# Optimization experiments

Hardware: AMD Instinct MI355X
Metric: run time of the kernel (lower is better)

The kernel has to match this reference:

```python
import jax, jax.numpy as jnp
import numpy as np

N_NODES = 50000
N_EDGES = 1_250_000
D_IN = 64
D_OUT = 64


def setup_inputs() -> dict:
    key = jax.random.key(0)
    k1, k2, k3, k4, k5 = jax.random.split(key, 5)
    feature = jax.random.normal(k1, (N_NODES, D_IN), dtype=jnp.float32)
    src = jax.random.randint(k2, (N_EDGES,), 0, N_NODES, dtype=jnp.int32)
    dst = jax.random.randint(k3, (N_EDGES,), 0, N_NODES, dtype=jnp.int32)
    W = jax.random.normal(k4, (D_OUT, D_IN), dtype=jnp.float32) * (1.0 / np.sqrt(D_IN))
    b = jax.random.normal(k5, (D_OUT,), dtype=jnp.float32) * 0.01
    return {"feature": feature, "src": src, "dst": dst, "W": W, "b": b}


def reference(feature, src, dst, W, b):
    # copy_u + sum: for each edge, message = feature[src]; reduce-sum at dst.
    msgs = feature[src]                                  # [E, D_IN] irregular gather
    h = jax.ops.segment_sum(msgs, dst, num_segments=N_NODES)  # [N, D_IN] scatter-add
    return h @ W.T + b                                   # nn.Linear
```

## Files before the change

### kernel.cpp

```cpp
#include <hip/hip_runtime.h>

#define D 64
#define SNB 256
#define CVB 128
#define NBP 1024
#define SCAP 5120
#define SLOTN 4608
#define GPAD 16
#define SLCAP 2048
#define VALID_LIM (1u<<22)
#define SCAN_CHUNK 1024

static __device__ __forceinline__ unsigned short f2bf(float f) {
    unsigned u = __float_as_uint(f);
    unsigned r = (u + 0x7FFFu + ((u >> 16) & 1u)) >> 16;
    return (unsigned short)r;
}
static __device__ __forceinline__ float bf2f(unsigned short h) {
    return __uint_as_float((unsigned)h << 16);
}

__global__ void __launch_bounds__(1024)
build2_kernel(const int* __restrict__ src, const int* __restrict__ dst,
              int* __restrict__ gcur, unsigned* __restrict__ pairs,
              const float* __restrict__ feature, unsigned short* __restrict__ fbf,
              int n_edges, int nb, int chunk, int n4) {
    if (blockIdx.x >= SNB) {
        int i = (blockIdx.x - SNB) * 1024 + threadIdx.x;
        for (; i < n4; i += CVB * 1024) {
            float4 v = ((const float4*)feature)[i];
            ushort4 r;
            r.x = f2bf(v.x); r.y = f2bf(v.y); r.z = f2bf(v.z); r.w = f2bf(v.w);
            ((ushort4*)fbf)[i] = r;
        }
        return;
    }

    __shared__ unsigned inb[SCAP];
    __shared__ unsigned sortedb[SCAP];
    __shared__ int hist[NBP];
    __shared__ int cur[NBP];
    __shared__ int dlt[NBP];
    __shared__ int pstart[NBP];
    __shared__ int pcnt[NBP];
    __shared__ int wsum[16];

    int blk = blockIdx.x, tid = threadIdx.x;
    int lane = tid & 63, w = tid >> 6;

    for (int i = tid; i < NBP; i += 1024) hist[i] = 0;
    __syncthreads();

    int e0 = blk * chunk;
    int e1 = e0 + chunk; if (e1 > n_edges) e1 = n_edges;
    int m = e1 - e0;

    for (int i = tid; i < m; i += 1024) {
        int d_ = dst[e0 + i];
        int s_ = src[e0 + i];
        inb[i] = ((unsigned)(d_ >> 6) << 22) | ((unsigned)(d_ & 63) << 16) | (unsigned)s_;
        atomicAdd(&hist[d_ >> 6], 1);
    }
    __syncthreads();

    int v = hist[tid];
    int x = v;
    for (int o = 1; o < 64; o <<= 1) {
        int y = __shfl_up(x, o, 64);
        if (lane >= o) x += y;
    }
    if (lane == 63) wsum[w] = x;
    __syncthreads();
    int pre = 0;
    for (int i = 0; i < w; ++i) pre += wsum[i];
    int excl = x - v + pre;
    cur[tid] = excl;
    if (tid < nb) {
        int res = (v + 15) & ~15;
        int gb = 0, okv = 0;
        if (v > 0) {
            gb = atomicAdd(&gcur[tid * GPAD], res);
            okv = (gb + res <= SLOTN) ? 1 : 0;
        }
        int bbase = tid * SLOTN;
        dlt[tid]    = okv ? (bbase + gb - excl) : (int)0x80000000;
        pstart[tid] = bbase + gb + v;
        pcnt[tid]   = okv ? (res - v) : 0;
    }
    __syncthreads();

    for (int i = tid; i < m; i += 1024) {
        unsigned p = inb[i];
        int pos = atomicAdd(&cur[p >> 22], 1);
        sortedb[pos] = p;
    }
    __syncthreads();

    for (int i = tid; i < m; i += 1024) {
        unsigned t = sortedb[i];
        int dl = dlt[t >> 22];
        if (dl != (int)0x80000000) pairs[dl + i] = t & 0x3FFFFFu;
    }
    for (int b = tid; b < nb; b += 1024) {
        int p0 = pstart[b], n = pcnt[b];
        for (int i = 0; i < n; ++i) pairs[p0 + i] = 0xFFFFFFFFu;
    }
}

__global__ void __launch_bounds__(1024, 8)
agg3_kernel(const unsigned short* __restrict__ fbf,
            const unsigned* __restrict__ pairs,
            const int* __restrict__ gcur,
            const float* __restrict__ W,
            const float* __restrict__ bias,
            float* __restrict__ out, int n_nodes) {
    __shared__ float4 Wt4[64 * 16];
    __shared__ float  H[64 * 65];
    __shared__ unsigned short slist[SLCAP];
    __shared__ int cnt[64], offs[64], cur[64];

    int tid = threadIdx.x;
    int lane = tid & 63, w = tid >> 6;
    int g = lane >> 4, sl = lane & 15;

    {   int k = tid >> 4, oq = tid & 15;
        float4 v;
        v.x = W[(4 * oq + 0) * 64 + k];
        v.y = W[(4 * oq + 1) * 64 + k];
        v.z = W[(4 * oq + 2) * 64 + k];
        v.w = W[(4 * oq + 3) * 64 + k];
        Wt4[k * 16 + oq] = v;
    }

    int bkt = blockIdx.x;
    int len = gcur[bkt * GPAD]; if (len > SLOTN) len = SLOTN;
    int e0 = bkt * SLOTN;

    if (tid < 64) cnt[tid] = 0;
    __syncthreads();
    for (int i = tid; i < len; i += 1024) {
        unsigned p = pairs[e0 + i];
        if (p < VALID_LIM) atomicAdd(&cnt[p >> 16], 1);
    }
    __syncthreads();
    if (w == 0) {
        int v = cnt[lane];
        int x = v;
        for (int o = 1; o < 64; o <<= 1) {
            int y = __shfl_up(x, o, 64);
            if (lane >= o) x += y;
        }
        offs[lane] = x - v; cur[lane] = x - v;
    }
    __syncthreads();
    for (int i = tid; i < len; i += 1024) {
        unsigned p = pairs[e0 + i];
        if (p < VALID_LIM) {
            int pos = atomicAdd(&cur[p >> 16], 1);
            if (pos < SLCAP) slist[pos] = (unsigned short)(p & 0xffffu);
        }
    }
    __syncthreads();

    int offq[4], dq[4];
#pragma unroll
    for (int q = 0; q < 4; ++q) {
        int ln = w + q * 16;
        offq[q] = offs[ln];
        dq[q] = cnt[ln];
    }
    int dmax = dq[0];
    if (dq[1] > dmax) dmax = dq[1];
    if (dq[2] > dmax) dmax = dq[2];
    if (dq[3] > dmax) dmax = dq[3];

    float4 a4[4];
#pragma unroll
    for (int q = 0; q < 4; ++q) { a4[q].x = a4[q].y = a4[q].z = a4[q].w = 0.f; }

    for (int j = 0; j < dmax; j += 4) {
        ushort4 u[4];
        float msk[4];
#pragma unroll
        for (int q = 0; q < 4; ++q) {
            int i0 = j + g;
            int d = dq[q];
            int ic = (i0 < d) ? i0 : ((d > 0) ? d - 1 : 0);
            int s = slist[offq[q] + ic];
            u[q] = *(const ushort4*)(fbf + s * D + sl * 4);
            msk[q] = (i0 < d) ? 1.f : 0.f;
        }
#pragma unroll
        for (int q = 0; q < 4; ++q) {
            a4[q].x += bf2f(u[q].x) * msk[q];
            a4[q].y += bf2f(u[q].y) * msk[q];
            a4[q].z += bf2f(u[q].z) * msk[q];
            a4[q].w += bf2f(u[q].w) * msk[q];
        }
    }

#pragma unroll
    for (int q = 0; q < 4; ++q) {
        float4 h = a4[q];
        h.x += __shfl_xor(h.x, 16, 64);  h.y += __shfl_xor(h.y, 16, 64);
        h.z += __shfl_xor(h.z, 16, 64);  h.w += __shfl_xor(h.w, 16, 64);
        h.x += __shfl_xor(h.x, 32, 64);  h.y += __shfl_xor(h.y, 32, 64);
        h.z += __shfl_xor(h.z, 32, 64);  h.w += __shfl_xor(h.w, 32, 64);
        if (g == 0) {
            int ln = w + q * 16;
            H[ln * 65 + sl * 4 + 0] = h.x;
            H[ln * 65 + sl * 4 + 1] = h.y;
            H[ln * 65 + sl * 4 + 2] = h.z;
            H[ln * 65 + sl * 4 + 3] = h.w;
        }
    }
    __syncthreads();

    int ln = tid >> 4, oq = tid & 15;
    int n = bkt * 64 + ln;
    if (n < n_nodes) {
        float4 r = *(const float4*)(bias + oq * 4);
#pragma unroll
        for (int k = 0; k < 64; ++k) {
            float hk = H[ln * 65 + k];
            float4 wv = Wt4[k * 16 + oq];
            r.x += hk * wv.x; r.y += hk * wv.y;
            r.z += hk * wv.z; r.w += hk * wv.w;
        }
        *(float4*)(out + n * D + oq * 4) = r;
    }
}


__global__ void hist_kernel(const int* __restrict__ dst, int* __restrict__ counts, int n_edges) {
    int e = blockIdx.x * blockDim.x + threadIdx.x;
    if (e < n_edges) atomicAdd(&counts[dst[e]], 1);
}

__global__ void reduce_kernel(const int* __restrict__ counts, int* __restrict__ partials, int n_nodes) {
    __shared__ int wsums[4];
    int tid = threadIdx.x;
    int base = blockIdx.x * SCAN_CHUNK + tid * 4;
    int s = 0;
#pragma unroll
    for (int i = 0; i < 4; ++i) {
        int idx = base + i;
        if (idx < n_nodes) s += counts[idx];
    }
    for (int o = 32; o > 0; o >>= 1) s += __shfl_down(s, o, 64);
    int lane = tid & 63, wave = tid >> 6;
    if (lane == 0) wsums[wave] = s;
    __syncthreads();
    if (tid == 0) partials[blockIdx.x] = wsums[0] + wsums[1] + wsums[2] + wsums[3];
}

__global__ void scan_partials_kernel(const int* __restrict__ partials, int* __restrict__ pscan, int nblk) {
    int lane = threadIdx.x;
    int v = (lane < nblk) ? partials[lane] : 0;
    int orig = v;
    for (int o = 1; o < 64; o <<= 1) {
        int y = __shfl_up(v, o, 64);
        if (lane >= o) v += y;
    }
    if (lane < nblk) pscan[lane] = v - orig;
}

__global__ void scan_kernel(const int* __restrict__ counts, const int* __restrict__ pscan,
                            int* __restrict__ offsets, int* __restrict__ cursors, int n_nodes) {
    __shared__ int wsums[4];
    int tid = threadIdx.x;
    int base = blockIdx.x * SCAN_CHUNK + tid * 4;
    int c[4];
    int tsum = 0;
#pragma unroll
    for (int i = 0; i < 4; ++i) {
        int idx = base + i;
        c[i] = (idx < n_nodes) ? counts[idx] : 0;
        tsum += c[i];
    }
    int lane = tid & 63, wave = tid >> 6;
    int x = tsum;
    for (int o = 1; o < 64; o <<= 1) {
        int y = __shfl_up(x, o, 64);
        if (lane >= o) x += y;
    }
    if (lane == 63) wsums[wave] = x;
    __syncthreads();
    int wpre = 0;
    for (int w = 0; w < wave; ++w) wpre += wsums[w];
    int excl = (x - tsum) + wpre + pscan[blockIdx.x];
#pragma unroll
    for (int i = 0; i < 4; ++i) {
        int idx = base + i;
        if (idx < n_nodes) { offsets[idx] = excl; cursors[idx] = excl; }
        excl += c[i];
    }
}

__global__ void fill_kernel(const int* __restrict__ src, const int* __restrict__ dst,
                            int* __restrict__ cursors, int* __restrict__ elist, int n_edges) {
    int e = blockIdx.x * blockDim.x + threadIdx.x;
    if (e < n_edges) {
        int pos = atomicAdd(&cursors[dst[e]], 1);
        elist[pos] = src[e];
    }
}

__global__ void agg_linear_kernel(const float* __restrict__ feature,
                                  const int* __restrict__ elist,
                                  const int* __restrict__ offsets,
                                  const int* __restrict__ counts,
                                  const float* __restrict__ W,
                                  const float* __restrict__ b,
                                  float* __restrict__ out,
                                  int n_nodes, int total_waves) {
    __shared__ float Wt[64 * 65];
    int tid = threadIdx.x;
    for (int i = tid; i < 64 * 64; i += 256) {
        int o = i >> 6, k = i & 63;
        Wt[k * 65 + o] = W[i];
    }
    __syncthreads();
    int lane = tid & 63;
    int waveId = (blockIdx.x * 256 + tid) >> 6;
    float bias = b[lane];
    for (int n = waveId; n < n_nodes; n += total_waves) {
        int off = offsets[n];
        int deg = counts[n];
        float acc = 0.f;
        int j = 0;
        for (; j + 4 <= deg; j += 4) {
            int s0 = elist[off + j + 0];
            int s1 = elist[off + j + 1];
            int s2 = elist[off + j + 2];
            int s3 = elist[off + j + 3];
            acc += feature[s0 * D + lane] + feature[s1 * D + lane]
                 + feature[s2 * D + lane] + feature[s3 * D + lane];
        }
        for (; j < deg; ++j) acc += feature[elist[off + j] * D + lane];
        float r = bias;
#pragma unroll
        for (int k = 0; k < 64; ++k) r += __shfl(acc, k, 64) * Wt[k * 65 + lane];
        out[n * D + lane] = r;
    }
}

__global__ void gcn_scatter_kernel(const float* __restrict__ feature,
                                   const int* __restrict__ src,
                                   const int* __restrict__ dst,
                                   float* __restrict__ out,
                                   int n_edges) {
    int e = blockIdx.x * 4 + (threadIdx.x >> 6);
    int lane = threadIdx.x & 63;
    if (e < n_edges) atomicAdd(&out[dst[e] * D + lane], feature[src[e] * D + lane]);
}

__global__ void gcn_linear_kernel(float* __restrict__ out,
                                  const float* __restrict__ W,
                                  const float* __restrict__ b,
                                  int n_nodes) {
    __shared__ float Wt[64 * 65];
    int tid = threadIdx.x;
    for (int i = tid; i < 64 * 64; i += 256) {
        int o = i >> 6, k = i & 63;
        Wt[k * 65 + o] = W[i];
    }
    __syncthreads();
    int lane = tid & 63;
    int n = blockIdx.x * 4 + (tid >> 6);
    if (n >= n_nodes) return;
    float val = out[n * D + lane];
    float acc = b[lane];
#pragma unroll
    for (int k = 0; k < 64; ++k) acc += __shfl(val, k, 64) * Wt[k * 65 + lane];
    out[n * D + lane] = acc;
}


extern "C" void kernel_launch(void* const* d_in, const int* in_sizes, int n_in,
                              void* d_out, int out_size, void* d_ws, size_t ws_size,
                              hipStream_t stream) {
    const float* feature = (const float*)d_in[0];
    const int* src       = (const int*)d_in[1];
    const int* dst       = (const int*)d_in[2];
    const float* W       = (const float*)d_in[3];
    const float* b       = (const float*)d_in[4];
    float* out           = (float*)d_out;

    int n_edges = in_sizes[1];
    int n_nodes = in_sizes[0] / D;

    int nb = (n_nodes + 63) >> 6;
    int chunk = (n_edges + SNB - 1) / SNB;
    int n4 = (n_nodes * D) / 4;

    size_t pairsWords = (size_t)nb * SLOTN;
    size_t needA = (size_t)NBP * GPAD * sizeof(int) + pairsWords * sizeof(int)
                 + (size_t)n_nodes * D * sizeof(unsigned short);

    if (n_nodes <= 65536 && nb <= NBP && chunk <= SCAP && ws_size >= needA) {
        int* gcur           = (int*)d_ws;
        unsigned* pairs     = (unsigned*)(gcur + (size_t)NBP * GPAD);
        unsigned short* fbf = (unsigned short*)(pairs + pairsWords);

        hipMemsetAsync(gcur, 0, (size_t)NBP * GPAD * sizeof(int), stream);
        build2_kernel<<<SNB + CVB, 1024, 0, stream>>>(src, dst, gcur, pairs,
                                                      feature, fbf,
                                                      n_edges, nb, chunk, n4);
        agg3_kernel<<<nb, 1024, 0, stream>>>(fbf, pairs, gcur, W, b, out, n_nodes);
        return;
    }

    size_t needB = ((size_t)3 * n_nodes + 128 + (size_t)n_edges) * sizeof(int);
    int nblk_scan = (n_nodes + SCAN_CHUNK - 1) / SCAN_CHUNK;
    if (ws_size >= needB && nblk_scan <= 64) {
        int* counts   = (int*)d_ws;
        int* offsets  = counts + n_nodes;
        int* cursors  = offsets + n_nodes;
        int* partials = cursors + n_nodes;
        int* pscan    = partials + 64;
        int* elist    = pscan + 64;

        hipMemsetAsync(counts, 0, (size_t)n_nodes * sizeof(int), stream);
        hist_kernel<<<(n_edges + 255) / 256, 256, 0, stream>>>(dst, counts, n_edges);
        reduce_kernel<<<nblk_scan, 256, 0, stream>>>(counts, partials, n_nodes);
        scan_partials_kernel<<<1, 64, 0, stream>>>(partials, pscan, nblk_scan);
        scan_kernel<<<nblk_scan, 256, 0, stream>>>(counts, pscan, offsets, cursors, n_nodes);
        fill_kernel<<<(n_edges + 255) / 256, 256, 0, stream>>>(src, dst, cursors, elist, n_edges);
        agg_linear_kernel<<<3125, 256, 0, stream>>>(feature, elist, offsets, counts, W, b, out,
                                                    n_nodes, 3125 * 4);
        return;
    }

    hipMemsetAsync(d_out, 0, (size_t)out_size * sizeof(float), stream);
    gcn_scatter_kernel<<<(n_edges + 3) / 4, 256, 0, stream>>>(feature, src, dst, out, n_edges);
    gcn_linear_kernel<<<(n_nodes + 3) / 4, 256, 0, stream>>>(out, W, b, n_nodes);
}
```

Baseline: 148.7 us.

## Scatter edge pairs directly via global atomics and halve aggregation block size

New measurement: 135.6 us. 8.8% less time.

```diff
diff --git a/kernel.cpp b/kernel.cpp
--- a/kernel.cpp
+++ b/kernel.cpp
@@ -5,10 +5,8 @@
 #define CVB 128
 #define NBP 1024
 #define SCAP 5120
-#define SLOTN 4608
+#define SLOTN 2048
 #define GPAD 16
-#define SLCAP 2048
-#define VALID_LIM (1u<<22)
 #define SCAN_CHUNK 1024
 
 static __device__ __forceinline__ unsigned short f2bf(float f) {
@@ -21,7 +19,7 @@
 }
 
 __global__ void __launch_bounds__(1024)
-build2_kernel(const int* __restrict__ src, const int* __restrict__ dst,
+build3_kernel(const int* __restrict__ src, const int* __restrict__ dst,
               int* __restrict__ gcur, unsigned* __restrict__ pairs,
               const float* __restrict__ feature, unsigned short* __restrict__ fbf,
               int n_edges, int nb, int chunk, int n4) {
@@ -37,16 +35,10 @@
     }
 
     __shared__ unsigned inb[SCAP];
-    __shared__ unsigned sortedb[SCAP];
     __shared__ int hist[NBP];
-    __shared__ int cur[NBP];
-    __shared__ int dlt[NBP];
-    __shared__ int pstart[NBP];
-    __shared__ int pcnt[NBP];
-    __shared__ int wsum[16];
+    __shared__ int gpos[NBP];
 
     int blk = blockIdx.x, tid = threadIdx.x;
-    int lane = tid & 63, w = tid >> 6;
 
     for (int i = tid; i < NBP; i += 1024) hist[i] = 0;
     __syncthreads();
@@ -63,52 +55,26 @@
     }
     __syncthreads();
 
-    int v = hist[tid];
-    int x = v;
-    for (int o = 1; o < 64; o <<= 1) {
-        int y = __shfl_up(x, o, 64);
-        if (lane >= o) x += y;
-    }
-    if (lane == 63) wsum[w] = x;
-    __syncthreads();
-    int pre = 0;
-    for (int i = 0; i < w; ++i) pre += wsum[i];
-    int excl = x - v + pre;
-    cur[tid] = excl;
     if (tid < nb) {
-        int res = (v + 15) & ~15;
-        int gb = 0, okv = 0;
+        int v = hist[tid];
         if (v > 0) {
-            gb = atomicAdd(&gcur[tid * GPAD], res);
-            okv = (gb + res <= SLOTN) ? 1 : 0;
-        }
-        int bbase = tid * SLOTN;
-        dlt[tid]    = okv ? (bbase + gb - excl) : (int)0x80000000;
-        pstart[tid] = bbase + gb + v;
-        pcnt[tid]   = okv ? (res - v) : 0;
+            int gb = atomicAdd(&gcur[tid * GPAD], v);
+            gpos[tid] = (gb + v <= SLOTN) ? (tid * SLOTN + gb) : (int)0x80000000;
+        } else {
+            gpos[tid] = (int)0x80000000;
+        }
     }
     __syncthreads();
 
     for (int i = tid; i < m; i += 1024) {
         unsigned p = inb[i];
-        int pos = atomicAdd(&cur[p >> 22], 1);
-        sortedb[pos] = p;
-    }
-    __syncthreads();
-
-    for (int i = tid; i < m; i += 1024) {
-        unsigned t = sortedb[i];
-        int dl = dlt[t >> 22];
-        if (dl != (int)0x80000000) pairs[dl + i] = t & 0x3FFFFFu;
-    }
-    for (int b = tid; b < nb; b += 1024) {
-        int p0 = pstart[b], n = pcnt[b];
-        for (int i = 0; i < n; ++i) pairs[p0 + i] = 0xFFFFFFFFu;
-    }
-}
-
-__global__ void __launch_bounds__(1024, 8)
-agg3_kernel(const unsigned short* __restrict__ fbf,
+        int pos = atomicAdd(&gpos[p >> 22], 1);
+        if (pos >= 0) pairs[pos] = p & 0x3FFFFFu;
+    }
+}
+
+__global__ void __launch_bounds__(512, 8)
+agg4_kernel(const unsigned short* __restrict__ fbf,
             const unsigned* __restrict__ pairs,
             const int* __restrict__ gcur,
             const float* __restrict__ W,
@@ -116,14 +82,17 @@
             float* __restrict__ out, int n_nodes) {
     __shared__ float4 Wt4[64 * 16];
     __shared__ float  H[64 * 65];
-    __shared__ unsigned short slist[SLCAP];
+    __shared__ unsigned short slist[SLOTN];
     __shared__ int cnt[64], offs[64], cur[64];
 
     int tid = threadIdx.x;
     int lane = tid & 63, w = tid >> 6;
     int g = lane >> 4, sl = lane & 15;
 
-    {   int k = tid >> 4, oq = tid & 15;
+#pragma unroll
+    for (int r = 0; r < 2; ++r) {
+        int item = tid + r * 512;
+        int k = item >> 4, oq = item & 15;
         float4 v;
         v.x = W[(4 * oq + 0) * 64 + k];
         v.y = W[(4 * oq + 1) * 64 + k];
@@ -138,10 +107,8 @@
 
     if (tid < 64) cnt[tid] = 0;
     __syncthreads();
-    for (int i = tid; i < len; i += 1024) {
-        unsigned p = pairs[e0 + i];
-        if (p < VALID_LIM) atomicAdd(&cnt[p >> 16], 1);
-    }
+    for (int i = tid; i < len; i += 512)
+        atomicAdd(&cnt[(pairs[e0 + i] >> 16) & 63], 1);
     __syncthreads();
     if (w == 0) {
         int v = cnt[lane];
@@ -153,81 +120,83 @@
         offs[lane] = x - v; cur[lane] = x - v;
     }
     __syncthreads();
-    for (int i = tid; i < len; i += 1024) {
+    for (int i = tid; i < len; i += 512) {
         unsigned p = pairs[e0 + i];
-        if (p < VALID_LIM) {
-            int pos = atomicAdd(&cur[p >> 16], 1);
-            if (pos < SLCAP) slist[pos] = (unsigned short)(p & 0xffffu);
-        }
-    }
-    __syncthreads();
-
-    int offq[4], dq[4];
-#pragma unroll
-    for (int q = 0; q < 4; ++q) {
-        int ln = w + q * 16;
-        offq[q] = offs[ln];
-        dq[q] = cnt[ln];
-    }
-    int dmax = dq[0];
-    if (dq[1] > dmax) dmax = dq[1];
-    if (dq[2] > dmax) dmax = dq[2];
-    if (dq[3] > dmax) dmax = dq[3];
-
-    float4 a4[4];
-#pragma unroll
-    for (int q = 0; q < 4; ++q) { a4[q].x = a4[q].y = a4[q].z = a4[q].w = 0.f; }
-
-    for (int j = 0; j < dmax; j += 4) {
-        ushort4 u[4];
-        float msk[4];
-#pragma unroll
-        for (int q = 0; q < 4; ++q) {
-            int i0 = j + g;
-            int d = dq[q];
-            int ic = (i0 < d) ? i0 : ((d > 0) ? d - 1 : 0);
-            int s = slist[offq[q] + ic];
-            u[q] = *(const ushort4*)(fbf + s * D + sl * 4);
-            msk[q] = (i0 < d) ? 1.f : 0.f;
-        }
-#pragma unroll
-        for (int q = 0; q < 4; ++q) {
-            a4[q].x += bf2f(u[q].x) * msk[q];
-            a4[q].y += bf2f(u[q].y) * msk[q];
-            a4[q].z += bf2f(u[q].z) * msk[q];
-            a4[q].w += bf2f(u[q].w) * msk[q];
-        }
-    }
-
-#pragma unroll
-    for (int q = 0; q < 4; ++q) {
-        float4 h = a4[q];
-        h.x += __shfl_xor(h.x, 16, 64);  h.y += __shfl_xor(h.y, 16, 64);
-        h.z += __shfl_xor(h.z, 16, 64);  h.w += __shfl_xor(h.w, 16, 64);
-        h.x += __shfl_xor(h.x, 32, 64);  h.y += __shfl_xor(h.y, 32, 64);
-        h.z += __shfl_xor(h.z, 32, 64);  h.w += __shfl_xor(h.w, 32, 64);
-        if (g == 0) {
-            int ln = w + q * 16;
-            H[ln * 65 + sl * 4 + 0] = h.x;
-            H[ln * 65 + sl * 4 + 1] = h.y;
-            H[ln * 65 + sl * 4 + 2] = h.z;
-            H[ln * 65 + sl * 4 + 3] = h.w;
-        }
-    }
-    __syncthreads();
-
-    int ln = tid >> 4, oq = tid & 15;
-    int n = bkt * 64 + ln;
-    if (n < n_nodes) {
-        float4 r = *(const float4*)(bias + oq * 4);
-#pragma unroll
-        for (int k = 0; k < 64; ++k) {
-            float hk = H[ln * 65 + k];
-            float4 wv = Wt4[k * 16 + oq];
-            r.x += hk * wv.x; r.y += hk * wv.y;
-            r.z += hk * wv.z; r.w += hk * wv.w;
-        }
-        *(float4*)(out + n * D + oq * 4) = r;
+        int pos = atomicAdd(&cur[(p >> 16) & 63], 1);
+        slist[pos] = (unsigned short)(p & 0xffffu);
+    }
+    __syncthreads();
+
+#pragma unroll
+    for (int qb = 0; qb < 2; ++qb) {
+        int offq[4], dq[4];
+        int dmax = 0;
+#pragma unroll
+        for (int qq = 0; qq < 4; ++qq) {
+            int ln = w + (qb * 4 + qq) * 8;
+            offq[qq] = offs[ln];
+            dq[qq] = cnt[ln];
+            if (dq[qq] > dmax) dmax = dq[qq];
+        }
+        float4 a4[4];
+#pragma unroll
+        for (int qq = 0; qq < 4; ++qq) { a4[qq].x = a4[qq].y = a4[qq].z = a4[qq].w = 0.f; }
+
+        for (int j = 0; j < dmax; j += 4) {
+            ushort4 u[4];
+            float msk[4];
+#pragma unroll
+            for (int qq = 0; qq < 4; ++qq) {
+                int i0 = j + g;
+                int d = dq[qq];
+                int ic = (i0 < d) ? i0 : ((d > 0) ? d - 1 : 0);
+                int s = slist[offq[qq] + ic];
+                u[qq] = *(const ushort4*)(fbf + s * D + sl * 4);
+                msk[qq] = (i0 < d) ? 1.f : 0.f;
+            }
+#pragma unroll
+            for (int qq = 0; qq < 4; ++qq) {
+                a4[qq].x += bf2f(u[qq].x) * msk[qq];
+                a4[qq].y += bf2f(u[qq].y) * msk[qq];
+                a4[qq].z += bf2f(u[qq].z) * msk[qq];
+                a4[qq].w += bf2f(u[qq].w) * msk[qq];
+            }
+        }
+
+#pragma unroll
+        for (int qq = 0; qq < 4; ++qq) {
+            float4 h = a4[qq];
+            h.x += __shfl_xor(h.x, 16, 64);  h.y += __shfl_xor(h.y, 16, 64);
+            h.z += __shfl_xor(h.z, 16, 64);  h.w += __shfl_xor(h.w, 16, 64);
+            h.x += __shfl_xor(h.x, 32, 64);  h.y += __shfl_xor(h.y, 32, 64);
+            h.z += __shfl_xor(h.z, 32, 64);  h.w += __shfl_xor(h.w, 32, 64);
+            if (g == 0) {
+                int ln = w + (qb * 4 + qq) * 8;
+                H[ln * 65 + sl * 4 + 0] = h.x;
+                H[ln * 65 + sl * 4 + 1] = h.y;
+                H[ln * 65 + sl * 4 + 2] = h.z;
+                H[ln * 65 + sl * 4 + 3] = h.w;
+            }
+        }
+    }
+    __syncthreads();
+
+#pragma unroll
+    for (int r = 0; r < 2; ++r) {
+        int item = tid + r * 512;
+        int ln = item >> 4, oq = item & 15;
+        int n = bkt * 64 + ln;
+        if (n < n_nodes) {
+            float4 rv = *(const float4*)(bias + oq * 4);
+#pragma unroll
+            for (int k = 0; k < 64; ++k) {
+                float hk = H[ln * 65 + k];
+                float4 wv = Wt4[k * 16 + oq];
+                rv.x += hk * wv.x; rv.y += hk * wv.y;
+                rv.z += hk * wv.z; rv.w += hk * wv.w;
+            }
+            *(float4*)(out + n * D + oq * 4) = rv;
+        }
     }
 }
 
@@ -404,10 +373,10 @@
         unsigned short* fbf = (unsigned short*)(pairs + pairsWords);
 
         hipMemsetAsync(gcur, 0, (size_t)NBP * GPAD * sizeof(int), stream);
-        build2_kernel<<<SNB + CVB, 1024, 0, stream>>>(src, dst, gcur, pairs,
+        build3_kernel<<<SNB + CVB, 1024, 0, stream>>>(src, dst, gcur, pairs,
                                                       feature, fbf,
                                                       n_edges, nb, chunk, n4);
-        agg3_kernel<<<nb, 1024, 0, stream>>>(fbf, pairs, gcur, W, b, out, n_nodes);
+        agg4_kernel<<<nb, 512, 0, stream>>>(fbf, pairs, gcur, W, b, out, n_nodes);
         return;
     }
 
```
